# Kernel tuning notes

Hardware: AMD Instinct MI355X
Metric: run time of the kernel (lower is better)

The kernel has to match this reference:

```python
import jax, jax.numpy as jnp
from jax import lax
import numpy as np

EPS = 1e-5

def lc2d(x, w, b, stride):
    # x: [B,H,W]; w: [oh,ow,kh,kw] unshared kernels; b: [oh,ow]
    oh, ow, kh, kw = w.shape
    hi = jnp.arange(oh)[:, None] * stride + jnp.arange(kh)[None, :]  # [oh,kh]
    wi = jnp.arange(ow)[:, None] * stride + jnp.arange(kw)[None, :]  # [ow,kw]
    patches = x[:, hi[:, None, :, None], wi[None, :, None, :]]  # [B,oh,ow,kh,kw]
    return jnp.einsum('bhwkl,hwkl->bhw', patches, w) + b

def ln2d(x, g, b):
    # LayerNorm over last two dims (per-sample)
    m = jnp.mean(x, axis=(-2, -1), keepdims=True)
    v = jnp.var(x, axis=(-2, -1), keepdims=True)
    return (x - m) * lax.rsqrt(v + EPS) * g + b

def maxpool2(x):
    # MaxPool2d(kernel=2, stride=2) on [B,H,W]
    return lax.reduce_window(x, -jnp.inf, lax.max, (1, 2, 2), (1, 2, 2), 'VALID')

def setup_inputs() -> dict:
    key = jax.random.key(0)
    ks = iter(jax.random.split(key, 16))
    d = {'x': jax.random.normal(next(ks), (128, 224, 224), jnp.float32)}
    layer_specs = [(109, 7), (50, 5), (48, 3), (22, 3), (20, 3), (8, 3)]
    for i, (o, k) in enumerate(layer_specs, 1):
        std = float(np.sqrt(2.0 / (k + k)))  # xavier_normal_ on a [k,k] kernel
        d[f'w{i}'] = jax.random.normal(next(ks), (o, o, k, k), jnp.float32) * std
        d[f'b{i}'] = jnp.zeros((o, o), jnp.float32)
        d[f'g{i}'] = jnp.ones((o, o), jnp.float32)
        d[f'be{i}'] = jnp.zeros((o, o), jnp.float32)
    d['fcw'] = jax.random.normal(next(ks), (1000, 64), jnp.float32) * float(np.sqrt(1.0 / 64))
    d['fcb'] = jnp.zeros((1000,), jnp.float32)
    return d

def reference(x, w1, b1, g1, be1, w2, b2, g2, be2, w3, b3, g3, be3,
              w4, b4, g4, be4, w5, b5, g5, be5, w6, b6, g6, be6, fcw, fcb):
    # dropout is inference-mode identity (p=0)
    h = ln2d(jax.nn.relu(lc2d(x, w1, b1, 2)), g1, be1)   # [B,109,109]
    h = maxpool2(h)                                       # [B,54,54]
    h = ln2d(jax.nn.relu(lc2d(h, w2, b2, 1)), g2, be2)   # [B,50,50]
    h = ln2d(jax.nn.relu(lc2d(h, w3, b3, 1)), g3, be3)   # [B,48,48]
    h = maxpool2(h)                                       # [B,24,24]
    h = ln2d(jax.nn.relu(lc2d(h, w4, b4, 1)), g4, be4)   # [B,22,22]
    h = ln2d(jax.nn.relu(lc2d(h, w5, b5, 1)), g5, be5)   # [B,20,20]
    h = maxpool2(h)                                       # [B,10,10]
    h = ln2d(jax.nn.relu(lc2d(h, w6, b6, 1)), g6, be6)   # [B,8,8]
    logits = h.reshape(h.shape[0], -1) @ fcw.T + fcb      # [B,1000]
    return jax.nn.softmax(logits, axis=1)
```

## Files before the change

### kernel.cpp

```cpp
#include <hip/hip_runtime.h>
#include <math.h>

static constexpr float kEps = 1e-5f;

__global__ __launch_bounds__(256)
void transpose_weights(const float* __restrict__ w1, const float* __restrict__ w2,
                       const float* __restrict__ w3, const float* __restrict__ w4,
                       const float* __restrict__ w5, const float* __restrict__ w6,
                       float* __restrict__ t1, float* __restrict__ t2,
                       float* __restrict__ t3, float* __restrict__ t4,
                       float* __restrict__ t5, float* __restrict__ t6)
{
    const int tid = blockIdx.x * blockDim.x + threadIdx.x;
    const int nt  = gridDim.x * blockDim.x;
    for (int i = tid; i < 49 * 109 * 112; i += nt) {
        const int kk = i / (109 * 112), r = i % (109 * 112);
        const int oh = r / 112, ow = r % 112;
        t1[i] = (ow < 109) ? w1[(oh * 109 + ow) * 49 + kk] : 0.f;
    }
    for (int i = tid; i < 25 * 50 * 52; i += nt) {
        const int kk = i / (50 * 52), r = i % (50 * 52);
        const int oh = r / 52, ow = r % 52;
        t2[i] = (ow < 50) ? w2[(oh * 50 + ow) * 25 + kk] : 0.f;
    }
    for (int i = tid; i < 9 * 2304; i += nt) {
        const int kk = i / 2304, idx = i % 2304;
        t3[i] = w3[idx * 9 + kk];
    }
    for (int i = tid; i < 9 * 22 * 24; i += nt) {
        const int kk = i / (22 * 24), r = i % (22 * 24);
        const int oh = r / 24, ow = r % 24;
        t4[i] = (ow < 22) ? w4[(oh * 22 + ow) * 9 + kk] : 0.f;
    }
    for (int i = tid; i < 9 * 400; i += nt) {
        const int kk = i / 400, idx = i % 400;
        t5[i] = w5[idx * 9 + kk];
    }
    for (int i = tid; i < 9 * 64; i += nt) {
        const int kk = i / 64, idx = i % 64;
        t6[i] = w6[idx * 9 + kk];
    }
}

__global__ __launch_bounds__(256)
void conv1(const float* __restrict__ x, const float* __restrict__ wt,
           const float* __restrict__ bias, float* __restrict__ y,
           float* __restrict__ partial)
{
    constexpr int IN = 224, OUT = 109, K = 7, RPS = 9, QPR = 28, NS = 13;
    __shared__ __align__(16) float xs0[23 * 224 + 8];
    __shared__ __align__(16) float xs1[23 * 224 + 8];
    __shared__ float red[4][4];

    const int s = blockIdx.x, bp = blockIdx.y, t = threadIdx.x;
    const int b0 = 2 * bp, b1 = b0 + 1;
    const int oh0 = s * RPS, ih0 = oh0 * 2;
    const int nrows = min(23, IN - ih0);
    {
        const float4* g0 = (const float4*)(x + ((size_t)b0 * IN + ih0) * IN);
        const float4* g1 = (const float4*)(x + ((size_t)b1 * IN + ih0) * IN);
        float4* s0 = (float4*)xs0;
        float4* s1 = (float4*)xs1;
        const int n4 = nrows * (IN / 4);
        for (int i = t; i < n4; i += 256) { s0[i] = g0[i]; s1[i] = g1[i]; }
    }
    __syncthreads();

    float lsum0 = 0.f, lsq0 = 0.f, lsum1 = 0.f, lsq1 = 0.f;
    if (t < RPS * QPR) {
        const int r = t / QPR, qc = t - r * QPR;
        const int oh = oh0 + r, ow0 = qc * 4;
        if (oh < OUT) {
            float acc0[4], acc1[4];
            #pragma unroll
            for (int o = 0; o < 4; ++o) {
                const float bv = (ow0 + o < OUT) ? bias[oh * OUT + ow0 + o] : 0.f;
                acc0[o] = bv; acc1[o] = bv;
            }
            const int lr0 = r * 2, c0 = ow0 * 2;
            #pragma unroll
            for (int kh = 0; kh < K; ++kh) {
                const float* p0 = xs0 + (lr0 + kh) * IN + c0;
                const float* p1 = xs1 + (lr0 + kh) * IN + c0;
                float a0[14], a1[14];
                #pragma unroll
                for (int i = 0; i < 7; ++i) {
                    const float2 v0 = *(const float2*)(p0 + 2 * i);
                    const float2 v1 = *(const float2*)(p1 + 2 * i);
                    a0[2 * i] = v0.x; a0[2 * i + 1] = v0.y;
                    a1[2 * i] = v1.x; a1[2 * i + 1] = v1.y;
                }
                #pragma unroll
                for (int kw = 0; kw < K; ++kw) {
                    const float4 w4 = *(const float4*)(wt + ((size_t)(kh * 7 + kw) * OUT + oh) * 112 + ow0);
                    acc0[0] = fmaf(a0[kw    ], w4.x, acc0[0]);  acc1[0] = fmaf(a1[kw    ], w4.x, acc1[0]);
                    acc0[1] = fmaf(a0[kw + 2], w4.y, acc0[1]);  acc1[1] = fmaf(a1[kw + 2], w4.y, acc1[1]);
                    acc0[2] = fmaf(a0[kw + 4], w4.z, acc0[2]);  acc1[2] = fmaf(a1[kw + 4], w4.z, acc1[2]);
                    acc0[3] = fmaf(a0[kw + 6], w4.w, acc0[3]);  acc1[3] = fmaf(a1[kw + 6], w4.w, acc1[3]);
                }
            }
            float4 st0, st1;
            #pragma unroll
            for (int o = 0; o < 4; ++o) {
                const float v0 = fmaxf(acc0[o], 0.f), v1 = fmaxf(acc1[o], 0.f);
                if (ow0 + o < OUT) {
                    lsum0 += v0; lsq0 = fmaf(v0, v0, lsq0);
                    lsum1 += v1; lsq1 = fmaf(v1, v1, lsq1);
                }
                (&st0.x)[o] = v0; (&st1.x)[o] = v1;
            }
            *(float4*)(y + ((size_t)b0 * OUT + oh) * 112 + ow0) = st0;
            *(float4*)(y + ((size_t)b1 * OUT + oh) * 112 + ow0) = st1;
        }
    }
    #pragma unroll
    for (int off = 32; off > 0; off >>= 1) {
        lsum0 += __shfl_down(lsum0, off, 64);  lsq0 += __shfl_down(lsq0, off, 64);
        lsum1 += __shfl_down(lsum1, off, 64);  lsq1 += __shfl_down(lsq1, off, 64);
    }
    if ((t & 63) == 0) {
        const int w = t >> 6;
        red[w][0] = lsum0; red[w][1] = lsq0; red[w][2] = lsum1; red[w][3] = lsq1;
    }
    __syncthreads();
    if (t == 0) {
        float a = 0, bq = 0, c = 0, d = 0;
        #pragma unroll
        for (int w = 0; w < 4; ++w) { a += red[w][0]; bq += red[w][1]; c += red[w][2]; d += red[w][3]; }
        partial[((size_t)b0 * NS + s) * 2]     = a;
        partial[((size_t)b0 * NS + s) * 2 + 1] = bq;
        partial[((size_t)b1 * NS + s) * 2]     = c;
        partial[((size_t)b1 * NS + s) * 2 + 1] = d;
    }
}

__device__ inline float2 block_stats(float lsum, float lsq, float invN,
                                     float (*red)[2], float* stat, int t)
{
    #pragma unroll
    for (int off = 32; off > 0; off >>= 1) {
        lsum += __shfl_down(lsum, off, 64);
        lsq  += __shfl_down(lsq,  off, 64);
    }
    if ((t & 63) == 0) { red[t >> 6][0] = lsum; red[t >> 6][1] = lsq; }
    __syncthreads();
    if (t == 0) {
        float s = 0, q = 0;
        #pragma unroll
        for (int w = 0; w < 4; ++w) { s += red[w][0]; q += red[w][1]; }
        const float m = s * invN;
        stat[0] = m;
        stat[1] = rsqrtf(q * invN - m * m + kEps);
    }
    __syncthreads();
    return make_float2(stat[0], stat[1]);
}

__global__ __launch_bounds__(256)
void tail(const float* __restrict__ y1, const float* __restrict__ partial,
          const float* __restrict__ g1, const float* __restrict__ be1,
          const float* __restrict__ w2t, const float* __restrict__ b2,
          const float* __restrict__ g2, const float* __restrict__ be2,
          const float* __restrict__ w3t, const float* __restrict__ b3,
          const float* __restrict__ g3, const float* __restrict__ be3,
          const float* __restrict__ w4t, const float* __restrict__ b4,
          const float* __restrict__ g4, const float* __restrict__ be4,
          const float* __restrict__ w5t, const float* __restrict__ b5,
          const float* __restrict__ g5, const float* __restrict__ be5,
          const float* __restrict__ w6t, const float* __restrict__ b6,
          const float* __restrict__ g6, const float* __restrict__ be6,
          const float* __restrict__ fcw, const float* __restrict__ fcb,
          float* __restrict__ out)
{
    __shared__ __align__(16) float xs54[54 * 54 + 8];
    __shared__ __align__(16) float y50[50 * 52];
    __shared__ __align__(16) float y48[48 * 48];
    __shared__ __align__(16) float xs24[24 * 24 + 8];
    __shared__ __align__(16) float y22[22 * 24];
    __shared__ __align__(16) float y20[20 * 20];
    __shared__ __align__(16) float xs10[100];
    __shared__ float y8[64], h[64];
    __shared__ float logits[1000];
    __shared__ float red[4][2];
    __shared__ float stat[2];

    const int b = blockIdx.x, t = threadIdx.x;

    if (t == 0) {
        float s = 0, q = 0;
        for (int i = 0; i < 13; ++i) {
            s += partial[((size_t)b * 13 + i) * 2];
            q += partial[((size_t)b * 13 + i) * 2 + 1];
        }
        const float m = s / 11881.f;
        stat[0] = m;
        stat[1] = rsqrtf(q / 11881.f - m * m + kEps);
    }
    __syncthreads();
    const float m1 = stat[0], r1 = stat[1];

    const float* yb = y1 + (size_t)b * 109 * 112;
    #pragma unroll
    for (int it = 0; it < 12; ++it) {
        const int idx = t + it * 256;
        if (idx < 54 * 54) {
            const int ph = idx / 54, pw = idx - ph * 54;
            const int r0 = 2 * ph, c0 = 2 * pw;
            const float2 u0 = *(const float2*)(yb + r0 * 112 + c0);
            const float2 u1 = *(const float2*)(yb + (r0 + 1) * 112 + c0);
            const int i00 = r0 * 109 + c0, i10 = i00 + 109;
            const float v0 = (u0.x - m1) * r1 * g1[i00]     + be1[i00];
            const float v1 = (u0.y - m1) * r1 * g1[i00 + 1] + be1[i00 + 1];
            const float v2 = (u1.x - m1) * r1 * g1[i10]     + be1[i10];
            const float v3 = (u1.y - m1) * r1 * g1[i10 + 1] + be1[i10 + 1];
            xs54[ph * 54 + pw] = fmaxf(fmaxf(v0, v1), fmaxf(v2, v3));
        }
    }
    __syncthreads();

    float ls = 0.f, lq = 0.f;
    #pragma unroll
    for (int it = 0; it < 3; ++it) {
        const int task = t + it * 256;
        if (task < 650) {
            const int oh = task / 13, qc = task - oh * 13;
            const int ow0 = qc * 4;
            float acc[4];
            #pragma unroll
            for (int o = 0; o < 4; ++o) acc[o] = (ow0 + o < 50) ? b2[oh * 50 + ow0 + o] : 0.f;
            #pragma unroll
            for (int kh = 0; kh < 5; ++kh) {
                const float* xp = xs54 + (oh + kh) * 54 + ow0;
                float a[8];
                #pragma unroll
                for (int i = 0; i < 4; ++i) {
                    const float2 v = *(const float2*)(xp + 2 * i);
                    a[2 * i] = v.x; a[2 * i + 1] = v.y;
                }
                #pragma unroll
                for (int kw = 0; kw < 5; ++kw) {
                    const float4 w4 = *(const float4*)(w2t + ((size_t)(kh * 5 + kw) * 50 + oh) * 52 + ow0);
                    acc[0] = fmaf(a[kw    ], w4.x, acc[0]);
                    acc[1] = fmaf(a[kw + 1], w4.y, acc[1]);
                    acc[2] = fmaf(a[kw + 2], w4.z, acc[2]);
                    acc[3] = fmaf(a[kw + 3], w4.w, acc[3]);
                }
            }
            #pragma unroll
            for (int o = 0; o < 4; ++o) {
                const float v = fmaxf(acc[o], 0.f);
                y50[oh * 52 + ow0 + o] = v;
                if (ow0 + o < 50) { ls += v; lq = fmaf(v, v, lq); }
            }
        }
    }
    const float2 s2 = block_stats(ls, lq, 1.f / 2500.f, red, stat, t);

    #pragma unroll
    for (int it = 0; it < 10; ++it) {
        const int idx = t + it * 256;
        if (idx < 2500) {
            const int oh = idx / 50, ow = idx - oh * 50;
            const int p = oh * 52 + ow;
            y50[p] = (y50[p] - s2.x) * s2.y * g2[idx] + be2[idx];
        }
    }
    __syncthreads();

    ls = 0.f; lq = 0.f;
    #pragma unroll
    for (int it = 0; it < 3; ++it) {
        const int task = t + it * 256;
        if (task < 576) {
            const int oh = task / 12, qc = task - oh * 12;
            const int ow0 = qc * 4;
            float acc[4];
            #pragma unroll
            for (int o = 0; o < 4; ++o) acc[o] = b3[oh * 48 + ow0 + o];
            #pragma unroll
            for (int kh = 0; kh < 3; ++kh) {
                const float* xp = y50 + (oh + kh) * 52 + ow0;
                float a[6];
                #pragma unroll
                for (int i = 0; i < 3; ++i) {
                    const float2 v = *(const float2*)(xp + 2 * i);
                    a[2 * i] = v.x; a[2 * i + 1] = v.y;
                }
                #pragma unroll
                for (int kw = 0; kw < 3; ++kw) {
                    const float4 w4 = *(const float4*)(w3t + (size_t)(kh * 3 + kw) * 2304 + oh * 48 + ow0);
                    acc[0] = fmaf(a[kw    ], w4.x, acc[0]);
                    acc[1] = fmaf(a[kw + 1], w4.y, acc[1]);
                    acc[2] = fmaf(a[kw + 2], w4.z, acc[2]);
                    acc[3] = fmaf(a[kw + 3], w4.w, acc[3]);
                }
            }
            float4 st;
            #pragma unroll
            for (int o = 0; o < 4; ++o) {
                const float v = fmaxf(acc[o], 0.f);
                (&st.x)[o] = v; ls += v; lq = fmaf(v, v, lq);
            }
            *(float4*)(y48 + oh * 48 + ow0) = st;
        }
    }
    const float2 s3 = block_stats(ls, lq, 1.f / 2304.f, red, stat, t);

    #pragma unroll
    for (int it = 0; it < 3; ++it) {
        const int idx = t + it * 256;
        if (idx < 576) {
            const int ph = idx / 24, pw = idx - ph * 24;
            const int r0 = 2 * ph, c0 = 2 * pw;
            const float2 u0 = *(const float2*)(y48 + r0 * 48 + c0);
            const float2 u1 = *(const float2*)(y48 + (r0 + 1) * 48 + c0);
            const int i00 = r0 * 48 + c0, i10 = i00 + 48;
            const float v0 = (u0.x - s3.x) * s3.y * g3[i00]     + be3[i00];
            const float v1 = (u0.y - s3.x) * s3.y * g3[i00 + 1] + be3[i00 + 1];
            const float v2 = (u1.x - s3.x) * s3.y * g3[i10]     + be3[i10];
            const float v3 = (u1.y - s3.x) * s3.y * g3[i10 + 1] + be3[i10 + 1];
            xs24[ph * 24 + pw] = fmaxf(fmaxf(v0, v1), fmaxf(v2, v3));
        }
    }
    __syncthreads();

    ls = 0.f; lq = 0.f;
    if (t < 132) {
        const int oh = t / 6, qc = t - oh * 6;
        const int ow0 = qc * 4;
        float acc[4];
        #pragma unroll
        for (int o = 0; o < 4; ++o) acc[o] = (ow0 + o < 22) ? b4[oh * 22 + ow0 + o] : 0.f;
        #pragma unroll
        for (int kh = 0; kh < 3; ++kh) {
            const float* xp = xs24 + (oh + kh) * 24 + ow0;
            float a[6];
            #pragma unroll
            for (int i = 0; i < 3; ++i) {
                const float2 v = *(const float2*)(xp + 2 * i);
                a[2 * i] = v.x; a[2 * i + 1] = v.y;
            }
            #pragma unroll
            for (int kw = 0; kw < 3; ++kw) {
                const float4 w4 = *(const float4*)(w4t + ((size_t)(kh * 3 + kw) * 22 + oh) * 24 + ow0);
                acc[0] = fmaf(a[kw    ], w4.x, acc[0]);
                acc[1] = fmaf(a[kw + 1], w4.y, acc[1]);
                acc[2] = fmaf(a[kw + 2], w4.z, acc[2]);
                acc[3] = fmaf(a[kw + 3], w4.w, acc[3]);
            }
        }
        #pragma unroll
        for (int o = 0; o < 4; ++o) {
            const float v = fmaxf(acc[o], 0.f);
            y22[oh * 24 + ow0 + o] = v;
            if (ow0 + o < 22) { ls += v; lq = fmaf(v, v, lq); }
        }
    }
    const float2 s4 = block_stats(ls, lq, 1.f / 484.f, red, stat, t);

    #pragma unroll
    for (int it = 0; it < 2; ++it) {
        const int idx = t + it * 256;
        if (idx < 484) {
            const int oh = idx / 22, ow = idx - oh * 22;
            const int p = oh * 24 + ow;
            y22[p] = (y22[p] - s4.x) * s4.y * g4[idx] + be4[idx];
        }
    }
    __syncthreads();

    ls = 0.f; lq = 0.f;
    if (t < 100) {
        const int oh = t / 5, qc = t - oh * 5;
        const int ow0 = qc * 4;
        float acc[4];
        #pragma unroll
        for (int o = 0; o < 4; ++o) acc[o] = b5[oh * 20 + ow0 + o];
        #pragma unroll
        for (int kh = 0; kh < 3; ++kh) {
            const float* xp = y22 + (oh + kh) * 24 + ow0;
            float a[6];
            #pragma unroll
            for (int i = 0; i < 3; ++i) {
                const float2 v = *(const float2*)(xp + 2 * i);
                a[2 * i] = v.x; a[2 * i + 1] = v.y;
            }
            #pragma unroll
            for (int kw = 0; kw < 3; ++kw) {
                const float4 w4 = *(const float4*)(w5t + (size_t)(kh * 3 + kw) * 400 + oh * 20 + ow0);
                acc[0] = fmaf(a[kw    ], w4.x, acc[0]);
                acc[1] = fmaf(a[kw + 1], w4.y, acc[1]);
                acc[2] = fmaf(a[kw + 2], w4.z, acc[2]);
                acc[3] = fmaf(a[kw + 3], w4.w, acc[3]);
            }
        }
        #pragma unroll
        for (int o = 0; o < 4; ++o) {
            const float v = fmaxf(acc[o], 0.f);
            y20[oh * 20 + ow0 + o] = v;
            ls += v; lq = fmaf(v, v, lq);
        }
    }
    const float2 s5 = block_stats(ls, lq, 1.f / 400.f, red, stat, t);

    if (t < 100) {
        const int ph = t / 10, pw = t - ph * 10;
        const int r0 = 2 * ph, c0 = 2 * pw;
        const float2 u0 = *(const float2*)(y20 + r0 * 20 + c0);
        const float2 u1 = *(const float2*)(y20 + (r0 + 1) * 20 + c0);
        const int i00 = r0 * 20 + c0, i10 = i00 + 20;
        const float v0 = (u0.x - s5.x) * s5.y * g5[i00]     + be5[i00];
        const float v1 = (u0.y - s5.x) * s5.y * g5[i00 + 1] + be5[i00 + 1];
        const float v2 = (u1.x - s5.x) * s5.y * g5[i10]     + be5[i10];
        const float v3 = (u1.y - s5.x) * s5.y * g5[i10 + 1] + be5[i10 + 1];
        xs10[ph * 10 + pw] = fmaxf(fmaxf(v0, v1), fmaxf(v2, v3));
    }
    __syncthreads();

    ls = 0.f; lq = 0.f;
    if (t < 16) {
        const int oh = t / 2, qc = t - oh * 2;
        const int ow0 = qc * 4;
        float acc[4];
        #pragma unroll
        for (int o = 0; o < 4; ++o) acc[o] = b6[oh * 8 + ow0 + o];
        #pragma unroll
        for (int kh = 0; kh < 3; ++kh) {
            const float* xp = xs10 + (oh + kh) * 10 + ow0;
            float a[6];
            #pragma unroll
            for (int i = 0; i < 3; ++i) {
                const float2 v = *(const float2*)(xp + 2 * i);
                a[2 * i] = v.x; a[2 * i + 1] = v.y;
            }
            #pragma unroll
            for (int kw = 0; kw < 3; ++kw) {
                const float4 w4 = *(const float4*)(w6t + (size_t)(kh * 3 + kw) * 64 + oh * 8 + ow0);
                acc[0] = fmaf(a[kw    ], w4.x, acc[0]);
                acc[1] = fmaf(a[kw + 1], w4.y, acc[1]);
                acc[2] = fmaf(a[kw + 2], w4.z, acc[2]);
                acc[3] = fmaf(a[kw + 3], w4.w, acc[3]);
            }
        }
        #pragma unroll
        for (int o = 0; o < 4; ++o) {
            const float v = fmaxf(acc[o], 0.f);
            y8[oh * 8 + ow0 + o] = v;
            ls += v; lq = fmaf(v, v, lq);
        }
    }
    const float2 s6 = block_stats(ls, lq, 1.f / 64.f, red, stat, t);

    if (t < 64) h[t] = (y8[t] - s6.x) * s6.y * g6[t] + be6[t];
    __syncthreads();

    #pragma unroll
    for (int it = 0; it < 4; ++it) {
        const int j = t + it * 256;
        if (j < 1000) {
            const float4* wr = (const float4*)(fcw + (size_t)j * 64);
            float acc = fcb[j];
            #pragma unroll
            for (int k = 0; k < 16; ++k) {
                const float4 w4 = wr[k];
                acc = fmaf(h[4 * k], w4.x,
                      fmaf(h[4 * k + 1], w4.y,
                      fmaf(h[4 * k + 2], w4.z,
                      fmaf(h[4 * k + 3], w4.w, acc))));
            }
            logits[j] = acc;
        }
    }
    __syncthreads();

    float lmax = -INFINITY;
    #pragma unroll
    for (int it = 0; it < 4; ++it) {
        const int j = t + it * 256;
        if (j < 1000) lmax = fmaxf(lmax, logits[j]);
    }
    #pragma unroll
    for (int off = 32; off > 0; off >>= 1) lmax = fmaxf(lmax, __shfl_down(lmax, off, 64));
    if ((t & 63) == 0) red[t >> 6][0] = lmax;
    __syncthreads();
    const float gmax = fmaxf(fmaxf(red[0][0], red[1][0]), fmaxf(red[2][0], red[3][0]));
    __syncthreads();
    float lsum = 0.f;
    #pragma unroll
    for (int it = 0; it < 4; ++it) {
        const int j = t + it * 256;
        if (j < 1000) {
            const float e = expf(logits[j] - gmax);
            logits[j] = e;
            lsum += e;
        }
    }
    #pragma unroll
    for (int off = 32; off > 0; off >>= 1) lsum += __shfl_down(lsum, off, 64);
    if ((t & 63) == 0) red[t >> 6][0] = lsum;
    __syncthreads();
    const float inv = 1.f / (red[0][0] + red[1][0] + red[2][0] + red[3][0]);
    #pragma unroll
    for (int it = 0; it < 4; ++it) {
        const int j = t + it * 256;
        if (j < 1000) out[(size_t)b * 1000 + j] = logits[j] * inv;
    }
}

extern "C" void kernel_launch(void* const* d_in, const int* in_sizes, int n_in,
                              void* d_out, int out_size, void* d_ws, size_t ws_size,
                              hipStream_t stream) {
    const float* x   = (const float*)d_in[0];
    const float* w1  = (const float*)d_in[1];
    const float* b1  = (const float*)d_in[2];
    const float* g1  = (const float*)d_in[3];
    const float* be1 = (const float*)d_in[4];
    const float* w2  = (const float*)d_in[5];
    const float* b2  = (const float*)d_in[6];
    const float* g2  = (const float*)d_in[7];
    const float* be2 = (const float*)d_in[8];
    const float* w3  = (const float*)d_in[9];
    const float* b3  = (const float*)d_in[10];
    const float* g3  = (const float*)d_in[11];
    const float* be3 = (const float*)d_in[12];
    const float* w4  = (const float*)d_in[13];
    const float* b4  = (const float*)d_in[14];
    const float* g4  = (const float*)d_in[15];
    const float* be4 = (const float*)d_in[16];
    const float* w5  = (const float*)d_in[17];
    const float* b5  = (const float*)d_in[18];
    const float* g5  = (const float*)d_in[19];
    const float* be5 = (const float*)d_in[20];
    const float* w6  = (const float*)d_in[21];
    const float* b6  = (const float*)d_in[22];
    const float* g6  = (const float*)d_in[23];
    const float* be6 = (const float*)d_in[24];
    const float* fcw = (const float*)d_in[25];
    const float* fcb = (const float*)d_in[26];

    float* y1p  = (float*)d_ws;
    float* w1t  = y1p  + 1562624;
    float* w2t  = w1t  + 598192;
    float* w3t  = w2t  + 65000;
    float* w4t  = w3t  + 20736;
    float* w5t  = w4t  + 4752;
    float* w6t  = w5t  + 3600;
    float* part = w6t  + 576;

    transpose_weights<<<512, 256, 0, stream>>>(w1, w2, w3, w4, w5, w6,
                                               w1t, w2t, w3t, w4t, w5t, w6t);

    conv1<<<dim3(13, 64), 256, 0, stream>>>(x, w1t, b1, y1p, part);

    tail<<<128, 256, 0, stream>>>(y1p, part, g1, be1,
                                  w2t, b2, g2, be2,
                                  w3t, b3, g3, be3,
                                  w4t, b4, g4, be4,
                                  w5t, b5, g5, be5,
                                  w6t, b6, g6, be6,
                                  fcw, fcb, (float*)d_out);
}
```

Measured before the change: 55.09 us.

## Retile conv1 into smaller row strips with more blocks and trim tail syncs

Conv1 now computes 4 output rows per block instead of 9, with 128 threads. The grid grows from 13x64 to 28x64, which uses more blocks across the CUs and less LDS per block. The aim is to fix the uneven last wave of blocks and improve occupancy, at the cost of re-loading more overlapping input rows. The tail kernel now reduces the 28 per-strip partial stats with a wave shuffle, drops one barrier from each LayerNorm stats step by having every thread read the shared partials directly, and uses __expf in the softmax.

```diff
diff --git a/kernel.cpp b/kernel.cpp
--- a/kernel.cpp
+++ b/kernel.cpp
@@ -42,27 +42,28 @@
     }
 }
 
-__global__ __launch_bounds__(256)
+__global__ __launch_bounds__(128)
 void conv1(const float* __restrict__ x, const float* __restrict__ wt,
            const float* __restrict__ bias, float* __restrict__ y,
            float* __restrict__ partial)
 {
-    constexpr int IN = 224, OUT = 109, K = 7, RPS = 9, QPR = 28, NS = 13;
-    __shared__ __align__(16) float xs0[23 * 224 + 8];
-    __shared__ __align__(16) float xs1[23 * 224 + 8];
-    __shared__ float red[4][4];
+    constexpr int IN = 224, OUT = 109, K = 7, RPS = 4, QPR = 28, NS = 28;
+    constexpr int ROWS = (RPS - 1) * 2 + K;
+    __shared__ __align__(16) float xs0[ROWS * IN];
+    __shared__ __align__(16) float xs1[ROWS * IN];
+    __shared__ float red[2][4];
 
     const int s = blockIdx.x, bp = blockIdx.y, t = threadIdx.x;
     const int b0 = 2 * bp, b1 = b0 + 1;
     const int oh0 = s * RPS, ih0 = oh0 * 2;
-    const int nrows = min(23, IN - ih0);
+    const int nrows = min(ROWS, IN - ih0);
     {
         const float4* g0 = (const float4*)(x + ((size_t)b0 * IN + ih0) * IN);
         const float4* g1 = (const float4*)(x + ((size_t)b1 * IN + ih0) * IN);
         float4* s0 = (float4*)xs0;
         float4* s1 = (float4*)xs1;
         const int n4 = nrows * (IN / 4);
-        for (int i = t; i < n4; i += 256) { s0[i] = g0[i]; s1[i] = g1[i]; }
+        for (int i = t; i < n4; i += 128) { s0[i] = g0[i]; s1[i] = g1[i]; }
     }
     __syncthreads();
 
@@ -124,9 +125,8 @@
     }
     __syncthreads();
     if (t == 0) {
-        float a = 0, bq = 0, c = 0, d = 0;
-        #pragma unroll
-        for (int w = 0; w < 4; ++w) { a += red[w][0]; bq += red[w][1]; c += red[w][2]; d += red[w][3]; }
+        const float a = red[0][0] + red[1][0], bq = red[0][1] + red[1][1];
+        const float c = red[0][2] + red[1][2], d  = red[0][3] + red[1][3];
         partial[((size_t)b0 * NS + s) * 2]     = a;
         partial[((size_t)b0 * NS + s) * 2 + 1] = bq;
         partial[((size_t)b1 * NS + s) * 2]     = c;
@@ -134,8 +134,8 @@
     }
 }
 
-__device__ inline float2 block_stats(float lsum, float lsq, float invN,
-                                     float (*red)[2], float* stat, int t)
+__device__ inline float2 block_stats4(float lsum, float lsq, float invN,
+                                      float (*red)[2], int t)
 {
     #pragma unroll
     for (int off = 32; off > 0; off >>= 1) {
@@ -144,16 +144,10 @@
     }
     if ((t & 63) == 0) { red[t >> 6][0] = lsum; red[t >> 6][1] = lsq; }
     __syncthreads();
-    if (t == 0) {
-        float s = 0, q = 0;
-        #pragma unroll
-        for (int w = 0; w < 4; ++w) { s += red[w][0]; q += red[w][1]; }
-        const float m = s * invN;
-        stat[0] = m;
-        stat[1] = rsqrtf(q * invN - m * m + kEps);
-    }
-    __syncthreads();
-    return make_float2(stat[0], stat[1]);
+    const float s = red[0][0] + red[1][0] + red[2][0] + red[3][0];
+    const float q = red[0][1] + red[1][1] + red[2][1] + red[3][1];
+    const float m = s * invN;
+    return make_float2(m, rsqrtf(q * invN - m * m + kEps));
 }
 
 __global__ __launch_bounds__(256)
@@ -172,6 +166,7 @@
           const float* __restrict__ fcw, const float* __restrict__ fcb,
           float* __restrict__ out)
 {
+    constexpr int NS = 28;
     __shared__ __align__(16) float xs54[54 * 54 + 8];
     __shared__ __align__(16) float y50[50 * 52];
     __shared__ __align__(16) float y48[48 * 48];
@@ -186,15 +181,24 @@
 
     const int b = blockIdx.x, t = threadIdx.x;
 
-    if (t == 0) {
-        float s = 0, q = 0;
-        for (int i = 0; i < 13; ++i) {
-            s += partial[((size_t)b * 13 + i) * 2];
-            q += partial[((size_t)b * 13 + i) * 2 + 1];
-        }
-        const float m = s / 11881.f;
-        stat[0] = m;
-        stat[1] = rsqrtf(q / 11881.f - m * m + kEps);
+    {
+        float s = 0.f, q = 0.f;
+        if (t < NS) {
+            const float2 p = *(const float2*)(partial + ((size_t)b * NS + t) * 2);
+            s = p.x; q = p.y;
+        }
+        if (t < 64) {
+            #pragma unroll
+            for (int off = 32; off > 0; off >>= 1) {
+                s += __shfl_down(s, off, 64);
+                q += __shfl_down(q, off, 64);
+            }
+            if (t == 0) {
+                const float m = s / 11881.f;
+                stat[0] = m;
+                stat[1] = rsqrtf(q / 11881.f - m * m + kEps);
+            }
+        }
     }
     __syncthreads();
     const float m1 = stat[0], r1 = stat[1];
@@ -254,7 +258,7 @@
             }
         }
     }
-    const float2 s2 = block_stats(ls, lq, 1.f / 2500.f, red, stat, t);
+    const float2 s2 = block_stats4(ls, lq, 1.f / 2500.f, red, t);
 
     #pragma unroll
     for (int it = 0; it < 10; ++it) {
@@ -304,7 +308,7 @@
             *(float4*)(y48 + oh * 48 + ow0) = st;
         }
     }
-    const float2 s3 = block_stats(ls, lq, 1.f / 2304.f, red, stat, t);
+    const float2 s3 = block_stats4(ls, lq, 1.f / 2304.f, red, t);
 
     #pragma unroll
     for (int it = 0; it < 3; ++it) {
@@ -356,7 +360,7 @@
             if (ow0 + o < 22) { ls += v; lq = fmaf(v, v, lq); }
         }
     }
-    const float2 s4 = block_stats(ls, lq, 1.f / 484.f, red, stat, t);
+    const float2 s4 = block_stats4(ls, lq, 1.f / 484.f, red, t);
 
     #pragma unroll
     for (int it = 0; it < 2; ++it) {
@@ -401,7 +405,7 @@
             ls += v; lq = fmaf(v, v, lq);
         }
     }
-    const float2 s5 = block_stats(ls, lq, 1.f / 400.f, red, stat, t);
+    const float2 s5 = block_stats4(ls, lq, 1.f / 400.f, red, t);
 
     if (t < 100) {
         const int ph = t / 10, pw = t - ph * 10;
@@ -449,7 +453,7 @@
             ls += v; lq = fmaf(v, v, lq);
         }
     }
-    const float2 s6 = block_stats(ls, lq, 1.f / 64.f, red, stat, t);
+    const float2 s6 = block_stats4(ls, lq, 1.f / 64.f, red, t);
 
     if (t < 64) h[t] = (y8[t] - s6.x) * s6.y * g6[t] + be6[t];
     __syncthreads();
@@ -490,7 +494,7 @@
     for (int it = 0; it < 4; ++it) {
         const int j = t + it * 256;
         if (j < 1000) {
-            const float e = expf(logits[j] - gmax);
+            const float e = __expf(logits[j] - gmax);
             logits[j] = e;
             lsum += e;
         }
@@ -550,7 +554,7 @@
     transpose_weights<<<512, 256, 0, stream>>>(w1, w2, w3, w4, w5, w6,
                                                w1t, w2t, w3t, w4t, w5t, w6t);
 
-    conv1<<<dim3(13, 64), 256, 0, stream>>>(x, w1t, b1, y1p, part);
+    conv1<<<dim3(28, 64), 128, 0, stream>>>(x, w1t, b1, y1p, part);
 
     tail<<<128, 256, 0, stream>>>(y1p, part, g1, be1,
                                   w2t, b2, g2, be2,
```

Measured after the change: 54.66 us. No clear change (-0.8%).
